# Kernel tuning notes

Measured on AMD Instinct MI355X. Metric: run time of the kernel, lower is better.

## Reference

```python
import jax, jax.numpy as jnp
import numpy as np

B, D, H, C, HALT_H, MAX_STEPS = 8192, 2048, 1024, 1000, 32, 10
EPS = 1e-08


def setup_inputs() -> dict:
    key = jax.random.key(0)
    ks = jax.random.split(key, 12)
    s = 0.02
    return {
        "x": jax.random.normal(ks[0], (B, D), jnp.float32),
        "enc_W": jax.random.normal(ks[1], (H, D), jnp.float32) * s,
        "enc_b": jnp.zeros((H,), jnp.float32),
        "ln_g": jnp.ones((H,), jnp.float32),
        "ln_b": jnp.zeros((H,), jnp.float32),
        "W_ih": jax.random.normal(ks[2], (3 * H, H), jnp.float32) * s,
        "W_hh": jax.random.normal(ks[3], (3 * H, H), jnp.float32) * s,
        "b_ih": jnp.zeros((3 * H,), jnp.float32),
        "b_hh": jnp.zeros((3 * H,), jnp.float32),
        "cls_W": jax.random.normal(ks[4], (C, H), jnp.float32) * s,
        "cls_b": jnp.zeros((C,), jnp.float32),
        "h1_W": jax.random.normal(ks[5], (HALT_H, H), jnp.float32) * s,
        "h1_b": jnp.zeros((HALT_H,), jnp.float32),
        "h2_W": jax.random.normal(ks[6], (1, HALT_H), jnp.float32) * s,
        "h2_b": jnp.zeros((1,), jnp.float32),
    }


def _forward(x, enc_W, enc_b, ln_g, ln_b, W_ih, W_hh, b_ih, b_hh,
             cls_W, cls_b, h1_W, h1_b, h2_W, h2_b):
    # encoder: Linear -> LayerNorm -> GELU (exact)
    z = x @ enc_W.T + enc_b
    mu = jnp.mean(z, axis=-1, keepdims=True)
    var = jnp.var(z, axis=-1, keepdims=True)
    z = (z - mu) * jax.lax.rsqrt(var + 1e-05) * ln_g + ln_b
    h0 = jax.nn.gelu(z, approximate=False)

    def step(h, _):
        gi = h @ W_ih.T + b_ih   # GRUCell with input = hidden
        gh = h @ W_hh.T + b_hh
        gi_r, gi_z, gi_n = jnp.split(gi, 3, axis=-1)
        gh_r, gh_z, gh_n = jnp.split(gh, 3, axis=-1)
        r = jax.nn.sigmoid(gi_r + gh_r)
        zt = jax.nn.sigmoid(gi_z + gh_z)
        n = jnp.tanh(gi_n + r * gh_n)
        h_new = (1.0 - zt) * n + zt * h
        logits = h_new @ cls_W.T + cls_b                         # [B, C]
        halt = jax.nn.sigmoid(
            jax.nn.relu(h_new @ h1_W.T + h1_b) @ h2_W.T + h2_b
        )[:, 0]                                                   # [B]
        return h_new, (logits, halt)

    _, (logits_steps, halt_steps) = jax.lax.scan(step, h0, None, length=MAX_STEPS)
    logits_stack = jnp.transpose(logits_steps, (1, 0, 2))  # [B, T, C]
    halts_stack = jnp.transpose(halt_steps, (1, 0))        # [B, T]

    log_not_halt = jnp.log(1.0 - halts_stack + EPS)
    cumsum_log = jnp.cumsum(log_not_halt, axis=1)
    cumsum_shifted = jnp.concatenate(
        [jnp.zeros((halts_stack.shape[0], 1), halts_stack.dtype), cumsum_log[:, :-1]], axis=1)
    halt_dist = halts_stack * jnp.exp(cumsum_shifted)
    remainder = 1.0 - jnp.sum(halt_dist, axis=1, keepdims=True)
    halt_dist = jnp.concatenate(
        [halt_dist[:, :-1], halt_dist[:, -1:] + jnp.maximum(remainder, 0.0)], axis=1)

    weighted_logits = jnp.sum(halt_dist[:, :, None] * logits_stack, axis=1)  # [B, C]
    step_indices = jnp.arange(1, MAX_STEPS + 1, dtype=weighted_logits.dtype)
    expected_steps = jnp.sum(halt_dist * step_indices, axis=1)
    probs = jax.nn.softmax(weighted_logits, axis=1)
    softmax_conf = jnp.max(probs, axis=1)
    comp_uncertainty = expected_steps / MAX_STEPS
    confidence = 0.7 * softmax_conf + 0.3 * (1.0 - comp_uncertainty)
    return (weighted_logits, probs, confidence, softmax_conf,
            expected_steps, halt_dist, comp_uncertainty)


def reference(x, enc_W, enc_b, ln_g, ln_b, W_ih, W_hh, b_ih, b_hh,
              cls_W, cls_b, h1_W, h1_b, h2_W, h2_b):
    return _forward(x, enc_W, enc_b, ln_g, ln_b, W_ih, W_hh, b_ih, b_hh,
                    cls_W, cls_b, h1_W, h1_b, h2_W, h2_b)
```

## Files before the change

kernel.cpp:

```cpp
#include <hip/hip_runtime.h>
#include <hip/hip_bf16.h>

#define B_ 8192
#define D_ 2048
#define H_ 1024
#define C_ 1000
#define NSTEP 10

typedef __attribute__((ext_vector_type(8))) short short8;
typedef __attribute__((ext_vector_type(4))) float f32x4;

__device__ __forceinline__ f32x4 mfma16x16(short8 a, short8 b, f32x4 c) {
  return __builtin_amdgcn_mfma_f32_16x16x32_bf16(a, b, c, 0, 0, 0);
}

__device__ __forceinline__ void async16(void* lds_uniform, const void* gsrc) {
  __builtin_amdgcn_global_load_lds(
      (const __attribute__((address_space(1))) void*)gsrc,
      (__attribute__((address_space(3))) void*)lds_uniform, 16, 0, 0);
}

__device__ __forceinline__ float sigm(float x) { return 1.0f / (1.0f + __expf(-x)); }
__device__ __forceinline__ float tanh_fast(float x) { return 1.0f - 2.0f / (__expf(2.0f * x) + 1.0f); }
__device__ __forceinline__ float b2f(short s) {
  union { unsigned u; float f; } v; v.u = ((unsigned)(unsigned short)s) << 16; return v.f;
}
__device__ __forceinline__ unsigned short f2us(float f) {
  __hip_bfloat16 h = __float2bfloat16(f); return *(unsigned short*)&h;
}

__device__ __forceinline__ int swz(int row, int slot) {
  return (row << 7) + (((slot) ^ (row & 7)) << 4);
}

__device__ __forceinline__ void halt_rows32(
    const __hip_bfloat16* __restrict__ hb, const __hip_bfloat16* __restrict__ h1Wb,
    const float* __restrict__ h1b, const float* __restrict__ h2W,
    const float* __restrict__ h2b, float* __restrict__ hbuf, int tcol,
    int m0base, float (*part)[2][64][8]) {
  const int tid = threadIdx.x, wave = tid >> 6, lane = tid & 63;
  const int rowgrp = wave >> 1, khalf = wave & 1;
  const int m0 = m0base + rowgrp * 16;
  const int lr = lane & 15, lk = (lane >> 4) * 8;

  const __hip_bfloat16* Arow = hb + (size_t)(m0 + lr) * H_ + khalf * 512 + lk;
  const __hip_bfloat16* B0 = h1Wb + (size_t)lr * H_ + khalf * 512 + lk;
  const __hip_bfloat16* B1 = h1Wb + (size_t)(16 + lr) * H_ + khalf * 512 + lk;
  f32x4 acc0 = {}, acc1 = {};
#pragma unroll 4
  for (int kk = 0; kk < 512; kk += 32) {
    short8 a  = *(const short8*)(Arow + kk);
    short8 b0 = *(const short8*)(B0 + kk);
    short8 b1 = *(const short8*)(B1 + kk);
    acc0 = mfma16x16(a, b0, acc0);
    acc1 = mfma16x16(a, b1, acc1);
  }
#pragma unroll
  for (int q = 0; q < 4; ++q) {
    part[rowgrp][khalf][lane][q]     = acc0[q];
    part[rowgrp][khalf][lane][4 + q] = acc1[q];
  }
  __syncthreads();
  if (!khalf) {
    const float w2a = h2W[lr], w2b = h2W[16 + lr];
    const float b1a = h1b[lr], b1b = h1b[16 + lr];
    float p[4];
#pragma unroll
    for (int q = 0; q < 4; ++q) {
      const float u0 = part[rowgrp][0][lane][q]     + part[rowgrp][1][lane][q]     + b1a;
      const float u1 = part[rowgrp][0][lane][4 + q] + part[rowgrp][1][lane][4 + q] + b1b;
      p[q] = fmaxf(u0, 0.f) * w2a + fmaxf(u1, 0.f) * w2b;
    }
#pragma unroll
    for (int m = 1; m < 16; m <<= 1) {
#pragma unroll
      for (int q = 0; q < 4; ++q) p[q] += __shfl_xor(p[q], m);
    }
    if (lr == 0) {
      const float b2 = h2b[0];
#pragma unroll
      for (int q = 0; q < 4; ++q) {
        const int row = m0 + (lane >> 4) * 4 + q;
        hbuf[(size_t)row * NSTEP + tcol] = 1.f / (1.f + expf(-(p[q] + b2)));
      }
    }
  }
  __syncthreads();
}

__global__ void cvt_all(const float* __restrict__ x, const float* __restrict__ encW,
                        const float* __restrict__ Wih, const float* __restrict__ Whh,
                        const float* __restrict__ clsW, const float* __restrict__ h1W,
                        __hip_bfloat16* __restrict__ xb, __hip_bfloat16* __restrict__ encWb,
                        __hip_bfloat16* __restrict__ Wc4b, __hip_bfloat16* __restrict__ clsWb,
                        __hip_bfloat16* __restrict__ h1Wb) {
  const int i = blockIdx.x * 256 + threadIdx.x;
  const int b0 = B_ * D_ / 4;
  const int b1 = b0 + H_ * D_ / 4;
  const int b2 = b1 + H_ * H_;
  const int b3 = b2 + 1024 * 1024 / 4;
  const int b4 = b3 + 32 * H_ / 4;
  if (i >= b4) return;
  float4 v;
  __hip_bfloat16* dst;
  int di;
  if (i < b0) {
    v = ((const float4*)x)[i]; dst = xb; di = i;
  } else if (i < b1) {
    const int j = i - b0;
    v = ((const float4*)encW)[j]; dst = encWb; di = j;
  } else if (i < b2) {
    const int j = i - b1;
    const int per_gate = H_ * H_ / 4;
    const int gate = j / per_gate, rem = j - gate * per_gate;
    if (gate == 0) {
      float4 a = ((const float4*)Wih)[rem], b = ((const float4*)Whh)[rem];
      v = make_float4(a.x + b.x, a.y + b.y, a.z + b.z, a.w + b.w);
    } else if (gate == 1) {
      float4 a = ((const float4*)Wih)[per_gate + rem], b = ((const float4*)Whh)[per_gate + rem];
      v = make_float4(a.x + b.x, a.y + b.y, a.z + b.z, a.w + b.w);
    } else if (gate == 2) {
      v = ((const float4*)Wih)[2 * per_gate + rem];
    } else {
      v = ((const float4*)Whh)[2 * per_gate + rem];
    }
    dst = Wc4b; di = j;
  } else if (i < b3) {
    const int j = i - b2;
    v = make_float4(0.f, 0.f, 0.f, 0.f);
    if (j < C_ * H_ / 4) v = ((const float4*)clsW)[j];
    dst = clsWb; di = j;
  } else {
    const int j = i - b3;
    v = ((const float4*)h1W)[j]; dst = h1Wb; di = j;
  }
  ((ushort4*)dst)[di] = make_ushort4(f2us(v.x), f2us(v.y), f2us(v.z), f2us(v.w));
}

template<int EPI>
__global__ __launch_bounds__(256, 2)
void gemm_bt(const __hip_bfloat16* __restrict__ A, int lda,
             const __hip_bfloat16* __restrict__ Bt, int ldb, int K,
             const float* __restrict__ bias,
             float* __restrict__ out, int out_ld, int ncol,
             const float* __restrict__ wrow) {
  __shared__ __hip_bfloat16 sA[128 * 64];
  __shared__ __hip_bfloat16 sB[128 * 64];
  const int tid = threadIdx.x;
  const int wave = tid >> 6, lane = tid & 63;
  const int m0 = blockIdx.x * 128, n0 = blockIdx.y * 128;
  const int wm = (wave >> 1) * 64, wn = (wave & 1) * 64;
  const int lr = lane & 15;
  const int g4 = lane >> 4;
  const int srow = wave * 8 + (lane >> 3);
  const int scol = ((lane & 7) ^ ((lane >> 3) & 7)) * 8;

  f32x4 acc[4][4] = {};

  const __hip_bfloat16* Asrc = A + (size_t)(m0 + srow) * lda + scol;
  const __hip_bfloat16* Bsrc = Bt + (size_t)(n0 + srow) * ldb + scol;

  for (int k0 = 0; k0 < K; k0 += 64) {
#pragma unroll
    for (int c = 0; c < 4; ++c) {
      async16((char*)sA + c * 4096 + wave * 1024, Asrc + (size_t)(c * 32) * lda + k0);
      async16((char*)sB + c * 4096 + wave * 1024, Bsrc + (size_t)(c * 32) * ldb + k0);
    }
    __syncthreads();
#pragma unroll
    for (int ks = 0; ks < 2; ++ks) {
      const int slot = ks * 4 + g4;
      short8 af[4], bfr[4];
#pragma unroll
      for (int i = 0; i < 4; ++i) {
        af[i]  = *(const short8*)((const char*)sA + swz(wm + i * 16 + lr, slot));
        bfr[i] = *(const short8*)((const char*)sB + swz(wn + i * 16 + lr, slot));
      }
#pragma unroll
      for (int i = 0; i < 4; ++i)
#pragma unroll
        for (int j = 0; j < 4; ++j)
          acc[i][j] = mfma16x16(af[i], bfr[j], acc[i][j]);
    }
    __syncthreads();
  }

  const int rbase = (lane >> 4) * 4;
  const int cbase = lane & 15;
#pragma unroll
  for (int i = 0; i < 4; ++i) {
#pragma unroll
    for (int r = 0; r < 4; ++r) {
      const int grow = m0 + wm + i * 16 + rbase + r;
      if (EPI == 1) {
        const float ws = wrow[grow];
#pragma unroll
        for (int j = 0; j < 4; ++j) {
          const int gcol = n0 + wn + j * 16 + cbase;
          if (gcol < ncol)
            out[(size_t)grow * out_ld + gcol] = acc[i][j][r] + bias[gcol] * ws;
        }
      } else {
#pragma unroll
        for (int j = 0; j < 4; ++j) {
          const int gcol = n0 + wn + j * 16 + cbase;
          out[(size_t)grow * out_ld + gcol] = acc[i][j][r] + bias[gcol];
        }
      }
    }
  }
}

__global__ __launch_bounds__(256, 2)
void gemm_gru(const __hip_bfloat16* __restrict__ A,
              const __hip_bfloat16* __restrict__ Wc4,
              const float* __restrict__ b_ih, const float* __restrict__ b_hh,
              __hip_bfloat16* __restrict__ hnewb,
              const __hip_bfloat16* __restrict__ h1Wb,
              const float* __restrict__ h1b, const float* __restrict__ h2W,
              const float* __restrict__ h2b, float* __restrict__ hbuf, int tcol) {
  __shared__ __hip_bfloat16 sA[128 * 64];
  __shared__ __hip_bfloat16 sB[4 * 64 * 64];
  if (blockIdx.y == 16) {
    if (tcol >= 0) {
      float (*part)[2][64][8] = (float (*)[2][64][8])sA;
      const int band = blockIdx.x * 128;
#pragma unroll
      for (int c = 0; c < 4; ++c)
        halt_rows32(A, h1Wb, h1b, h2W, h2b, hbuf, tcol, band + c * 32, part);
    }
    return;
  }
  const int tid = threadIdx.x, wave = tid >> 6, lane = tid & 63;
  const int m0 = blockIdx.x * 128, n0 = blockIdx.y * 64;
  const int wr = wave >> 1, wc = wave & 1;
  const int lr = lane & 15;
  const int g4 = lane >> 4;
  const int srow = lane >> 3;
  const int scol = ((lane & 7) ^ ((lane >> 3) & 7)) * 8;

  f32x4 acc[4][4][2] = {};

  const __hip_bfloat16* Asrc = A + (size_t)(m0 + wave * 8 + srow) * H_ + scol;
  const __hip_bfloat16* Bsrc = Wc4 + (size_t)(n0 + wave * 8 + srow) * H_ + scol;

  for (int k0 = 0; k0 < H_; k0 += 64) {
#pragma unroll
    for (int c = 0; c < 4; ++c)
      async16((char*)sA + c * 4096 + wave * 1024, Asrc + (size_t)(c * 32) * H_ + k0);
#pragma unroll
    for (int g = 0; g < 4; ++g)
#pragma unroll
      for (int d = 0; d < 2; ++d)
        async16((char*)sB + g * 8192 + d * 4096 + wave * 1024,
                Bsrc + ((size_t)g << 20) + (size_t)(d * 32) * H_ + k0);
    __syncthreads();
#pragma unroll
    for (int ks = 0; ks < 2; ++ks) {
      const int slot = ks * 4 + g4;
      short8 af[4];
#pragma unroll
      for (int mi = 0; mi < 4; ++mi)
        af[mi] = *(const short8*)((const char*)sA + swz(wr * 64 + mi * 16 + lr, slot));
      short8 bf[4][2];
#pragma unroll
      for (int g = 0; g < 4; ++g)
#pragma unroll
        for (int hb = 0; hb < 2; ++hb)
          bf[g][hb] = *(const short8*)((const char*)sB + g * 8192
                                       + swz(wc * 32 + hb * 16 + lr, slot));
#pragma unroll
      for (int mi = 0; mi < 4; ++mi)
#pragma unroll
        for (int g = 0; g < 4; ++g)
#pragma unroll
          for (int hb = 0; hb < 2; ++hb)
            acc[mi][g][hb] = mfma16x16(af[mi], bf[g][hb], acc[mi][g][hb]);
    }
    __syncthreads();
  }

  const int rbase = (lane >> 4) * 4;
  const int cbase = lane & 15;
#pragma unroll
  for (int hb = 0; hb < 2; ++hb) {
    const int gcol = n0 + wc * 32 + hb * 16 + cbase;
    const float brz = b_ih[gcol] + b_hh[gcol];
    const float bzz = b_ih[H_ + gcol] + b_hh[H_ + gcol];
    const float bin = b_ih[2 * H_ + gcol];
    const float bhn = b_hh[2 * H_ + gcol];
#pragma unroll
    for (int mi = 0; mi < 4; ++mi) {
#pragma unroll
      for (int r = 0; r < 4; ++r) {
        const int grow = m0 + wr * 64 + mi * 16 + rbase + r;
        const size_t idx = (size_t)grow * H_ + gcol;
        const float rg = sigm(acc[mi][0][hb][r] + brz);
        const float zg = sigm(acc[mi][1][hb][r] + bzz);
        const float ng = tanh_fast(acc[mi][2][hb][r] + bin + rg * (acc[mi][3][hb][r] + bhn));
        const float hv = b2f(*(const short*)(A + idx));
        hnewb[idx] = __float2bfloat16((1.0f - zg) * ng + zg * hv);
      }
    }
  }
}

__global__ __launch_bounds__(256, 4)
void halt_last(const __hip_bfloat16* __restrict__ hb,
               const __hip_bfloat16* __restrict__ h1Wb,
               const float* __restrict__ h1b, const float* __restrict__ h2W,
               const float* __restrict__ h2b, float* __restrict__ hbuf, int tcol) {
  __shared__ float part[2][2][64][8];
  halt_rows32(hb, h1Wb, h1b, h2W, h2b, hbuf, tcol, blockIdx.x * 32, part);
}

__global__ void ln_gelu(const float* __restrict__ z, const float* __restrict__ g,
                        const float* __restrict__ bta, __hip_bfloat16* __restrict__ hb) {
  const int row = blockIdx.x, t = threadIdx.x;
  __shared__ float rs[4], rs2[4];
  float4 v = ((const float4*)(z + (size_t)row * H_))[t];
  float s = v.x + v.y + v.z + v.w;
  float s2 = v.x * v.x + v.y * v.y + v.z * v.z + v.w * v.w;
#pragma unroll
  for (int off = 32; off; off >>= 1) {
    s += __shfl_down(s, off);
    s2 += __shfl_down(s2, off);
  }
  if ((t & 63) == 0) { rs[t >> 6] = s; rs2[t >> 6] = s2; }
  __syncthreads();
  const float mu = (rs[0] + rs[1] + rs[2] + rs[3]) * (1.0f / H_);
  const float var = (rs2[0] + rs2[1] + rs2[2] + rs2[3]) * (1.0f / H_) - mu * mu;
  const float rstd = rsqrtf(var + 1e-5f);
  float4 gg = ((const float4*)g)[t];
  float4 bb = ((const float4*)bta)[t];
  float o[4], res[4];
  o[0] = (v.x - mu) * rstd * gg.x + bb.x;
  o[1] = (v.y - mu) * rstd * gg.y + bb.y;
  o[2] = (v.z - mu) * rstd * gg.z + bb.z;
  o[3] = (v.w - mu) * rstd * gg.w + bb.w;
#pragma unroll
  for (int k = 0; k < 4; ++k)
    res[k] = 0.5f * o[k] * (1.0f + erff(o[k] * 0.70710678118654752f));
  ((ushort4*)(hb + (size_t)row * H_))[t] =
      make_ushort4(f2us(res[0]), f2us(res[1]), f2us(res[2]), f2us(res[3]));
}

__global__ void ponder_rec(const float* __restrict__ hbuf,
                           float* __restrict__ out_hd, float* __restrict__ out_es,
                           float* __restrict__ out_cu, float* __restrict__ wsum) {
  const int row = blockIdx.x * 256 + threadIdx.x;
  const float* hp = hbuf + (size_t)row * NSTEP;
  float c = 0.f, ps = 0.f, es = 0.f;
  float hd[NSTEP];
#pragma unroll
  for (int t = 0; t < NSTEP; ++t) {
    const float halt = hp[t];
    const float pt = halt * expf(c);
    float w;
    if (t == NSTEP - 1) {
      w = pt + fmaxf(1.f - (ps + pt), 0.f);
    } else {
      w = pt;
      c += logf(1.f - halt + 1e-8f);
      ps += pt;
    }
    es += w * (float)(t + 1);
    hd[t] = w;
  }
#pragma unroll
  for (int t = 0; t < NSTEP; ++t) out_hd[(size_t)row * NSTEP + t] = hd[t];
  out_es[row] = es;
  out_cu[row] = es * (1.0f / NSTEP);
  wsum[row] = ps + hd[NSTEP - 1];
}

__global__ void hw_final(const __hip_bfloat16* __restrict__ hstack,
                         const float* __restrict__ out_hd,
                         __hip_bfloat16* __restrict__ hwb) {
  const int t = threadIdx.x;
  const int row = blockIdx.x * 4 + (t >> 6);
  const int c0 = (t & 63) * 16;
  const float* hd = out_hd + (size_t)row * NSTEP;
  float accv[16] = {};
#pragma unroll
  for (int s = 0; s < NSTEP; ++s) {
    const float w = hd[s];
    const short8* p = (const short8*)(hstack + ((size_t)(s + 1) * B_ + row) * H_ + c0);
    short8 a0 = p[0], a1 = p[1];
#pragma unroll
    for (int q = 0; q < 8; ++q) accv[q] += w * b2f(a0[q]);
#pragma unroll
    for (int q = 0; q < 8; ++q) accv[8 + q] += w * b2f(a1[q]);
  }
  short8 r0, r1;
#pragma unroll
  for (int q = 0; q < 8; ++q) { r0[q] = (short)f2us(accv[q]); r1[q] = (short)f2us(accv[8 + q]); }
  short8* dst = (short8*)(hwb + (size_t)row * H_ + c0);
  dst[0] = r0; dst[1] = r1;
}

__global__ void finalize(const float* __restrict__ wl, const float* __restrict__ es,
                         float* __restrict__ probs, float* __restrict__ conf,
                         float* __restrict__ sconf) {
  const int row = blockIdx.x, t = threadIdx.x;
  __shared__ float red[4], red2[4];
  float4 v = make_float4(-1e30f, -1e30f, -1e30f, -1e30f);
  float m = -1e30f;
  if (t < 250) {
    v = ((const float4*)(wl + (size_t)row * C_))[t];
    m = fmaxf(fmaxf(v.x, v.y), fmaxf(v.z, v.w));
  }
#pragma unroll
  for (int off = 32; off; off >>= 1) m = fmaxf(m, __shfl_down(m, off));
  if ((t & 63) == 0) red[t >> 6] = m;
  __syncthreads();
  m = fmaxf(fmaxf(red[0], red[1]), fmaxf(red[2], red[3]));
  float4 e = make_float4(0.f, 0.f, 0.f, 0.f);
  float s = 0.f;
  if (t < 250) {
    e.x = expf(v.x - m); e.y = expf(v.y - m); e.z = expf(v.z - m); e.w = expf(v.w - m);
    s = e.x + e.y + e.z + e.w;
  }
#pragma unroll
  for (int off = 32; off; off >>= 1) s += __shfl_down(s, off);
  if ((t & 63) == 0) red2[t >> 6] = s;
  __syncthreads();
  s = red2[0] + red2[1] + red2[2] + red2[3];
  const float inv = 1.0f / s;
  if (t < 250)
    ((float4*)(probs + (size_t)row * C_))[t] = make_float4(e.x * inv, e.y * inv, e.z * inv, e.w * inv);
  if (t == 0) {
    sconf[row] = inv;
    conf[row] = 0.7f * inv + 0.3f * (1.0f - es[row] * (1.0f / NSTEP));
  }
}

extern "C" void kernel_launch(void* const* d_in, const int* in_sizes, int n_in,
                              void* d_out, int out_size, void* d_ws, size_t ws_size,
                              hipStream_t stream) {
  (void)in_sizes; (void)n_in; (void)out_size; (void)ws_size;
  const float* x     = (const float*)d_in[0];
  const float* enc_W = (const float*)d_in[1];
  const float* enc_b = (const float*)d_in[2];
  const float* ln_g  = (const float*)d_in[3];
  const float* ln_b  = (const float*)d_in[4];
  const float* W_ih  = (const float*)d_in[5];
  const float* W_hh  = (const float*)d_in[6];
  const float* b_ih  = (const float*)d_in[7];
  const float* b_hh  = (const float*)d_in[8];
  const float* cls_W = (const float*)d_in[9];
  const float* cls_b = (const float*)d_in[10];
  const float* h1_W  = (const float*)d_in[11];
  const float* h1_b  = (const float*)d_in[12];
  const float* h2_W  = (const float*)d_in[13];
  const float* h2_b  = (const float*)d_in[14];

  char* wsp = (char*)d_ws;
  auto carve = [&](size_t n) { char* p = wsp; wsp += (n + 255) & ~(size_t)255; return p; };
  __hip_bfloat16* Wc4b   = (__hip_bfloat16*)carve((size_t)4 * H_ * H_ * 2);
  __hip_bfloat16* clsWb  = (__hip_bfloat16*)carve((size_t)1024 * 1024 * 2);
  __hip_bfloat16* encWb  = (__hip_bfloat16*)carve((size_t)H_ * D_ * 2);
  __hip_bfloat16* h1Wb   = (__hip_bfloat16*)carve((size_t)32 * H_ * 2);
  __hip_bfloat16* hstack = (__hip_bfloat16*)carve((size_t)(NSTEP + 1) * B_ * H_ * 2);
  float* wsum = (float*)carve((size_t)B_ * 4);
  float* hbuf = (float*)carve((size_t)B_ * NSTEP * 4);

  const size_t SLOT = (size_t)B_ * H_;
  float* z            = (float*)(hstack + SLOT);
  __hip_bfloat16* xb  = hstack + 3 * SLOT;
  __hip_bfloat16* hwb = hstack;

  float* out = (float*)d_out;
  float* out_wl    = out;
  float* out_probs = out + (size_t)B_ * C_;
  float* out_conf  = out + (size_t)2 * B_ * C_;
  float* out_sconf = out_conf + B_;
  float* out_es    = out_sconf + B_;
  float* out_hd    = out_es + B_;
  float* out_cu    = out_hd + (size_t)B_ * NSTEP;

  dim3 blk(256);
  {
    const int total = B_ * D_ / 4 + H_ * D_ / 4 + H_ * H_ + 1024 * 1024 / 4 + 32 * H_ / 4;
    cvt_all<<<(total + 255) / 256, blk, 0, stream>>>(
        x, enc_W, W_ih, W_hh, cls_W, h1_W, xb, encWb, Wc4b, clsWb, h1Wb);
  }

  gemm_bt<0><<<dim3(B_ / 128, H_ / 128), blk, 0, stream>>>(
      xb, D_, encWb, D_, D_, enc_b, z, H_, H_, nullptr);
  ln_gelu<<<B_, blk, 0, stream>>>(z, ln_g, ln_b, hstack);

  for (int step = 0; step < NSTEP; ++step) {
    const __hip_bfloat16* hprev = hstack + (size_t)step * SLOT;
    __hip_bfloat16* hnext = hstack + (size_t)(step + 1) * SLOT;
    gemm_gru<<<dim3(B_ / 128, 17), blk, 0, stream>>>(
        hprev, Wc4b, b_ih, b_hh, hnext, h1Wb, h1_b, h2_W, h2_b, hbuf, step - 1);
  }
  halt_last<<<B_ / 32, blk, 0, stream>>>(
      hstack + (size_t)NSTEP * SLOT, h1Wb, h1_b, h2_W, h2_b, hbuf, NSTEP - 1);

  ponder_rec<<<B_ / 256, blk, 0, stream>>>(hbuf, out_hd, out_es, out_cu, wsum);

  hw_final<<<B_ / 4, blk, 0, stream>>>(hstack, out_hd, hwb);

  gemm_bt<1><<<dim3(B_ / 128, 1024 / 128), blk, 0, stream>>>(
      hwb, H_, clsWb, H_, H_, cls_b, out_wl, C_, C_, wsum);

  finalize<<<B_, blk, 0, stream>>>(out_wl, out_es, out_probs, out_conf, out_sconf);
}
```

Baseline: 1.058 ms.

## Move halting MLP out of GRU step kernels into one batched launch

The halting-head MLP used to run in an extra blockIdx.y row of each GRU step kernel, with a separate launch for the last step. It now runs in one kernel over all steps (grid over row bands × steps) after the recurrence finishes, reading every hidden state from hstack. This takes the halting work off the serial critical path of the recurrence and drops the extra launch, but the hidden states must be re-read from memory and the work no longer overlaps with the GEMM tail.

```diff
diff --git a/kernel.cpp b/kernel.cpp
--- a/kernel.cpp
+++ b/kernel.cpp
@@ -31,61 +31,6 @@
 
 __device__ __forceinline__ int swz(int row, int slot) {
   return (row << 7) + (((slot) ^ (row & 7)) << 4);
-}
-
-__device__ __forceinline__ void halt_rows32(
-    const __hip_bfloat16* __restrict__ hb, const __hip_bfloat16* __restrict__ h1Wb,
-    const float* __restrict__ h1b, const float* __restrict__ h2W,
-    const float* __restrict__ h2b, float* __restrict__ hbuf, int tcol,
-    int m0base, float (*part)[2][64][8]) {
-  const int tid = threadIdx.x, wave = tid >> 6, lane = tid & 63;
-  const int rowgrp = wave >> 1, khalf = wave & 1;
-  const int m0 = m0base + rowgrp * 16;
-  const int lr = lane & 15, lk = (lane >> 4) * 8;
-
-  const __hip_bfloat16* Arow = hb + (size_t)(m0 + lr) * H_ + khalf * 512 + lk;
-  const __hip_bfloat16* B0 = h1Wb + (size_t)lr * H_ + khalf * 512 + lk;
-  const __hip_bfloat16* B1 = h1Wb + (size_t)(16 + lr) * H_ + khalf * 512 + lk;
-  f32x4 acc0 = {}, acc1 = {};
-#pragma unroll 4
-  for (int kk = 0; kk < 512; kk += 32) {
-    short8 a  = *(const short8*)(Arow + kk);
-    short8 b0 = *(const short8*)(B0 + kk);
-    short8 b1 = *(const short8*)(B1 + kk);
-    acc0 = mfma16x16(a, b0, acc0);
-    acc1 = mfma16x16(a, b1, acc1);
-  }
-#pragma unroll
-  for (int q = 0; q < 4; ++q) {
-    part[rowgrp][khalf][lane][q]     = acc0[q];
-    part[rowgrp][khalf][lane][4 + q] = acc1[q];
-  }
-  __syncthreads();
-  if (!khalf) {
-    const float w2a = h2W[lr], w2b = h2W[16 + lr];
-    const float b1a = h1b[lr], b1b = h1b[16 + lr];
-    float p[4];
-#pragma unroll
-    for (int q = 0; q < 4; ++q) {
-      const float u0 = part[rowgrp][0][lane][q]     + part[rowgrp][1][lane][q]     + b1a;
-      const float u1 = part[rowgrp][0][lane][4 + q] + part[rowgrp][1][lane][4 + q] + b1b;
-      p[q] = fmaxf(u0, 0.f) * w2a + fmaxf(u1, 0.f) * w2b;
-    }
-#pragma unroll
-    for (int m = 1; m < 16; m <<= 1) {
-#pragma unroll
-      for (int q = 0; q < 4; ++q) p[q] += __shfl_xor(p[q], m);
-    }
-    if (lr == 0) {
-      const float b2 = h2b[0];
-#pragma unroll
-      for (int q = 0; q < 4; ++q) {
-        const int row = m0 + (lane >> 4) * 4 + q;
-        hbuf[(size_t)row * NSTEP + tcol] = 1.f / (1.f + expf(-(p[q] + b2)));
-      }
-    }
-  }
-  __syncthreads();
 }
 
 __global__ void cvt_all(const float* __restrict__ x, const float* __restrict__ encW,
@@ -215,22 +160,9 @@
 void gemm_gru(const __hip_bfloat16* __restrict__ A,
               const __hip_bfloat16* __restrict__ Wc4,
               const float* __restrict__ b_ih, const float* __restrict__ b_hh,
-              __hip_bfloat16* __restrict__ hnewb,
-              const __hip_bfloat16* __restrict__ h1Wb,
-              const float* __restrict__ h1b, const float* __restrict__ h2W,
-              const float* __restrict__ h2b, float* __restrict__ hbuf, int tcol) {
+              __hip_bfloat16* __restrict__ hnewb) {
   __shared__ __hip_bfloat16 sA[128 * 64];
   __shared__ __hip_bfloat16 sB[4 * 64 * 64];
-  if (blockIdx.y == 16) {
-    if (tcol >= 0) {
-      float (*part)[2][64][8] = (float (*)[2][64][8])sA;
-      const int band = blockIdx.x * 128;
-#pragma unroll
-      for (int c = 0; c < 4; ++c)
-        halt_rows32(A, h1Wb, h1b, h2W, h2b, hbuf, tcol, band + c * 32, part);
-    }
-    return;
-  }
   const int tid = threadIdx.x, wave = tid >> 6, lane = tid & 63;
   const int m0 = blockIdx.x * 128, n0 = blockIdx.y * 64;
   const int wr = wave >> 1, wc = wave & 1;
@@ -303,15 +235,6 @@
       }
     }
   }
-}
-
-__global__ __launch_bounds__(256, 4)
-void halt_last(const __hip_bfloat16* __restrict__ hb,
-               const __hip_bfloat16* __restrict__ h1Wb,
-               const float* __restrict__ h1b, const float* __restrict__ h2W,
-               const float* __restrict__ h2b, float* __restrict__ hbuf, int tcol) {
-  __shared__ float part[2][2][64][8];
-  halt_rows32(hb, h1Wb, h1b, h2W, h2b, hbuf, tcol, blockIdx.x * 32, part);
 }
 
 __global__ void ln_gelu(const float* __restrict__ z, const float* __restrict__ g,
@@ -343,6 +266,64 @@
     res[k] = 0.5f * o[k] * (1.0f + erff(o[k] * 0.70710678118654752f));
   ((ushort4*)(hb + (size_t)row * H_))[t] =
       make_ushort4(f2us(res[0]), f2us(res[1]), f2us(res[2]), f2us(res[3]));
+}
+
+__global__ __launch_bounds__(256, 4)
+void halt_mlp_all(const __hip_bfloat16* __restrict__ hstack,
+                  const __hip_bfloat16* __restrict__ h1Wb,
+                  const float* __restrict__ h1b, const float* __restrict__ h2W,
+                  const float* __restrict__ h2b,
+                  float* __restrict__ hbuf) {
+  __shared__ float part[2][2][64][8];
+  const int tid = threadIdx.x, wave = tid >> 6, lane = tid & 63;
+  const int tstep = blockIdx.y;
+  const __hip_bfloat16* hb = hstack + (size_t)(tstep + 1) * B_ * H_;
+  const int rowgrp = wave >> 1, khalf = wave & 1;
+  const int m0 = (blockIdx.x * 2 + rowgrp) * 16;
+  const int lr = lane & 15, lk = (lane >> 4) * 8;
+
+  const __hip_bfloat16* Arow = hb + (size_t)(m0 + lr) * H_ + khalf * 512 + lk;
+  const __hip_bfloat16* B0 = h1Wb + (size_t)lr * H_ + khalf * 512 + lk;
+  const __hip_bfloat16* B1 = h1Wb + (size_t)(16 + lr) * H_ + khalf * 512 + lk;
+  f32x4 acc0 = {}, acc1 = {};
+#pragma unroll 4
+  for (int kk = 0; kk < 512; kk += 32) {
+    short8 a  = *(const short8*)(Arow + kk);
+    short8 b0 = *(const short8*)(B0 + kk);
+    short8 b1 = *(const short8*)(B1 + kk);
+    acc0 = mfma16x16(a, b0, acc0);
+    acc1 = mfma16x16(a, b1, acc1);
+  }
+#pragma unroll
+  for (int q = 0; q < 4; ++q) {
+    part[rowgrp][khalf][lane][q]     = acc0[q];
+    part[rowgrp][khalf][lane][4 + q] = acc1[q];
+  }
+  __syncthreads();
+  if (khalf) return;
+
+  const float w2a = h2W[lr], w2b = h2W[16 + lr];
+  const float b1a = h1b[lr], b1b = h1b[16 + lr];
+  float p[4];
+#pragma unroll
+  for (int q = 0; q < 4; ++q) {
+    const float u0 = part[rowgrp][0][lane][q]     + part[rowgrp][1][lane][q]     + b1a;
+    const float u1 = part[rowgrp][0][lane][4 + q] + part[rowgrp][1][lane][4 + q] + b1b;
+    p[q] = fmaxf(u0, 0.f) * w2a + fmaxf(u1, 0.f) * w2b;
+  }
+#pragma unroll
+  for (int m = 1; m < 16; m <<= 1) {
+#pragma unroll
+    for (int q = 0; q < 4; ++q) p[q] += __shfl_xor(p[q], m);
+  }
+  if (lr == 0) {
+    const float b2 = h2b[0];
+#pragma unroll
+    for (int q = 0; q < 4; ++q) {
+      const int row = m0 + (lane >> 4) * 4 + q;
+      hbuf[(size_t)row * NSTEP + tstep] = 1.f / (1.f + expf(-(p[q] + b2)));
+    }
+  }
 }
 
 __global__ void ponder_rec(const float* __restrict__ hbuf,
@@ -493,12 +474,12 @@
   for (int step = 0; step < NSTEP; ++step) {
     const __hip_bfloat16* hprev = hstack + (size_t)step * SLOT;
     __hip_bfloat16* hnext = hstack + (size_t)(step + 1) * SLOT;
-    gemm_gru<<<dim3(B_ / 128, 17), blk, 0, stream>>>(
-        hprev, Wc4b, b_ih, b_hh, hnext, h1Wb, h1_b, h2_W, h2_b, hbuf, step - 1);
-  }
-  halt_last<<<B_ / 32, blk, 0, stream>>>(
-      hstack + (size_t)NSTEP * SLOT, h1Wb, h1_b, h2_W, h2_b, hbuf, NSTEP - 1);
-
+    gemm_gru<<<dim3(B_ / 128, H_ / 64), blk, 0, stream>>>(
+        hprev, Wc4b, b_ih, b_hh, hnext);
+  }
+
+  halt_mlp_all<<<dim3(B_ / 32, NSTEP), blk, 0, stream>>>(
+      hstack, h1Wb, h1_b, h2_W, h2_b, hbuf);
   ponder_rec<<<B_ / 256, blk, 0, stream>>>(hbuf, out_hd, out_es, out_cu, wsum);
 
   hw_final<<<B_ / 4, blk, 0, stream>>>(hstack, out_hd, hwb);
```

Measured after the change: 899.0 us. -15.1%, faster.
